# Optimization experiments

Measured on AMD Instinct MI355X. Metric: run time of the kernel, lower is better.

The kernel has to match this reference:

```python
import math
import jax, jax.numpy as jnp
from jax import lax
import numpy as np

B, M, L = 256, 21, 512
P, S, D = 16, 8, 256
NL, EXP, H, LAM = 3, 2, 96, 0.01
T = (L - P) // S + 1  # 63 patches
HID = D * EXP


def _pos_enc():
    pe = np.zeros((T, D), np.float32)
    pos = np.arange(T, dtype=np.float32)[:, None]
    div = np.exp(np.arange(0, D, 2, dtype=np.float32) * (-math.log(10000.0) / D))
    pe[:, 0::2] = np.sin(pos * div)
    pe[:, 1::2] = np.cos(pos * div)
    return jnp.asarray(pe)


def _clin(zr, zi, Wr, Wi, br, bi):
    # faithful to torch: bias br added to both terms of yr (cancels), bi added twice in yi
    yr = (zr @ Wr.T + br) - (zi @ Wi.T + br)
    yi = (zr @ Wi.T + bi) + (zi @ Wr.T + bi)
    return yr, yi


def _softshrink(zr, zi):
    mag = jnp.sqrt(zr * zr + zi * zi)
    scale = jnp.maximum(mag - LAM, 0.0) / (mag + 1e-8) * (mag > LAM).astype(zr.dtype)
    return zr * scale, zi * scale


def _layernorm(x, g, b):
    mu = jnp.mean(x, -1, keepdims=True)
    var = jnp.mean((x - mu) ** 2, -1, keepdims=True)
    return (x - mu) / jnp.sqrt(var + 1e-5) * g + b


def _block(x, p):
    (Tw, Tb, Gew, Geb, Gpw, Gpb,
     H1Wr, H1Wi, H1br, H1bi, H2Wr, H2Wi, H2br, H2bi, lng, lnb) = p
    g = jax.nn.gelu(x @ Gew.T + Geb, approximate=False) @ Gpw.T + Gpb
    zf = jnp.fft.rfft(x, axis=1)  # FFT along time/patch axis T
    zr, zi = zf.real, zf.imag
    zr, zi = _clin(zr, zi, H1Wr, H1Wi, H1br, H1bi)
    zr, zi = _softshrink(zr, zi)
    zr, zi = _clin(zr, zi, H2Wr, H2Wi, H2br, H2bi)
    pt = jnp.fft.irfft(lax.complex(zr, zi), n=x.shape[1], axis=1)
    out = (g * pt) @ Tw.T + Tb
    return _layernorm(out + x, lng, lnb)


def _forward(x, conv_w, conv_b, tp, sp, gate_w, gate_b, proj_w, proj_b):
    # per-instance, per-variable norm over time (biased std, eps on std)
    mean = jnp.mean(x, -1, keepdims=True)
    std = jnp.sqrt(jnp.mean((x - mean) ** 2, -1, keepdims=True))
    xn = (x - mean) / (std + 1e-5)
    patches = lax.conv_general_dilated(xn, conv_w, (S,), 'VALID',
                                       dimension_numbers=('NCH', 'OIH', 'NCH'))
    patches = patches + conv_b[None, :, None]
    h = patches.transpose(0, 2, 1) + _pos_enc()[None]  # (B, T, D)
    t = h
    s = h
    for i in range(NL):
        t = _block(t, tuple(a[i] for a in tp))
        s = _block(s, tuple(a[i] for a in sp))
    gate = jax.nn.sigmoid(t @ gate_w.T + gate_b)
    feat = gate * t + (1.0 - gate) * s
    out = feat.reshape(feat.shape[0], -1) @ proj_w.T + proj_b
    y = out.reshape(-1, M, H) * (std + 1e-5) + mean
    return y


def setup_inputs() -> dict:
    key = jax.random.key(0)
    ks = iter(jax.random.split(key, 64))

    def nrm(shape, scale):
        return jax.random.normal(next(ks), shape, jnp.float32) * scale

    inp = {'x': nrm((B, M, L), 1.0)}
    inp['conv_w'] = nrm((D, M, P), 1.0 / math.sqrt(M * P))
    inp['conv_b'] = jnp.zeros((D,), jnp.float32)

    def layer_params(prefix):
        d = {}
        d[prefix + 'Tw'] = nrm((NL, D, D), 1.0 / math.sqrt(D))
        d[prefix + 'Tb'] = jnp.zeros((NL, D), jnp.float32)
        d[prefix + 'Gew'] = nrm((NL, HID, D), 1.0 / math.sqrt(D))
        d[prefix + 'Geb'] = jnp.zeros((NL, HID), jnp.float32)
        d[prefix + 'Gpw'] = nrm((NL, D, HID), 1.0 / math.sqrt(HID))
        d[prefix + 'Gpb'] = jnp.zeros((NL, D), jnp.float32)
        for hname in ('H1', 'H2'):
            d[prefix + hname + 'Wr'] = nrm((NL, D, D), 1.0 / math.sqrt(D))
            d[prefix + hname + 'Wi'] = nrm((NL, D, D), 1.0 / math.sqrt(D))
            d[prefix + hname + 'br'] = jnp.zeros((NL, D), jnp.float32)
            d[prefix + hname + 'bi'] = jnp.zeros((NL, D), jnp.float32)
        d[prefix + 'lng'] = jnp.ones((NL, D), jnp.float32)
        d[prefix + 'lnb'] = jnp.zeros((NL, D), jnp.float32)
        return d

    inp.update(layer_params('t_'))
    inp.update(layer_params('s_'))
    inp['gate_w'] = nrm((1, D), 1.0 / math.sqrt(D))
    inp['gate_b'] = jnp.zeros((1,), jnp.float32)
    inp['proj_w'] = nrm((M * H, T * D), 1.0 / math.sqrt(T * D))
    inp['proj_b'] = jnp.zeros((M * H,), jnp.float32)
    return inp


def reference(x, conv_w, conv_b,
              t_Tw, t_Tb, t_Gew, t_Geb, t_Gpw, t_Gpb,
              t_H1Wr, t_H1Wi, t_H1br, t_H1bi, t_H2Wr, t_H2Wi, t_H2br, t_H2bi, t_lng, t_lnb,
              s_Tw, s_Tb, s_Gew, s_Geb, s_Gpw, s_Gpb,
              s_H1Wr, s_H1Wi, s_H1br, s_H1bi, s_H2Wr, s_H2Wi, s_H2br, s_H2bi, s_lng, s_lnb,
              gate_w, gate_b, proj_w, proj_b):
    tp = (t_Tw, t_Tb, t_Gew, t_Geb, t_Gpw, t_Gpb,
          t_H1Wr, t_H1Wi, t_H1br, t_H1bi, t_H2Wr, t_H2Wi, t_H2br, t_H2bi, t_lng, t_lnb)
    sp = (s_Tw, s_Tb, s_Gew, s_Geb, s_Gpw, s_Gpb,
          s_H1Wr, s_H1Wi, s_H1br, s_H1bi, s_H2Wr, s_H2Wi, s_H2br, s_H2bi, s_lng, s_lnb)
    return _forward(x, conv_w, conv_b, tp, sp, gate_w, gate_b, proj_w, proj_b)
```

## Files before the change

kernel.cpp:

```cpp
#include <hip/hip_runtime.h>
#include <cstddef>
#include <cstdint>

#define B_    256
#define M_    21
#define L_    512
#define D_    256
#define T_    63
#define F_    32
#define NT_   16128
#define HID_  512
#define KCP_  352
#define H_    96
#define LAM_  0.01f
#define PZ_   16

typedef __attribute__((ext_vector_type(8))) short short8;
typedef __attribute__((ext_vector_type(4))) float f32x4;
typedef unsigned int u32;
typedef const u32 __attribute__((address_space(1)))* gas1_t;
typedef u32 __attribute__((address_space(3)))* las3_t;

__device__ __forceinline__ void async_copy16(const void* g, void* l) {
  __builtin_amdgcn_global_load_lds((gas1_t)g, (las3_t)(uintptr_t)l, 16, 0, 0);
}
__device__ __forceinline__ unsigned short f2bf(float x) {
  unsigned u = __float_as_uint(x);
  return (unsigned short)((u + 0x7FFF + ((u >> 16) & 1)) >> 16);
}
__device__ __forceinline__ float bf2f(unsigned short u) {
  return __uint_as_float(((unsigned)u) << 16);
}
__device__ __forceinline__ float gelu_exact(float v) {
  return 0.5f * v * (1.0f + erff(v * 0.70710678118654752f));
}
__device__ __forceinline__ float block_sum256(float v, float* red4) {
  #pragma unroll
  for (int off = 32; off > 0; off >>= 1) v += __shfl_down(v, off, 64);
  if ((threadIdx.x & 63) == 0) red4[threadIdx.x >> 6] = v;
  __syncthreads();
  float r = red4[0] + red4[1] + red4[2] + red4[3];
  __syncthreads();
  return r;
}
__device__ __forceinline__ float wave_sum(float v) {
  #pragma unroll
  for (int off = 1; off < 64; off <<= 1) v += __shfl_xor(v, off, 64);
  return v;
}

struct CvtEnt { const float* src; unsigned short* dst; int rows, scol, dcol, blk0; };
struct CvtArgs { CvtEnt e[19]; int nent; };
__global__ __launch_bounds__(256) void wprep_kernel(CvtArgs a) {
  int blk = blockIdx.x, e = 0;
  while (e + 1 < a.nent && a.e[e + 1].blk0 <= blk) ++e;
  CvtEnt en = a.e[e];
  int idx = (blk - en.blk0) * 256 + threadIdx.x;
  int total = en.rows * en.dcol;
  if (idx >= total) return;
  int r = idx / en.dcol, c = idx - r * en.dcol;
  float v = (c < en.scol) ? en.src[(size_t)r * en.scol + c] : 0.f;
  en.dst[idx] = f2bf(v);
}

struct CatArgs { const float* wr[12]; const float* wi[12]; };
__global__ __launch_bounds__(256) void wcat_kernel(CatArgs a, unsigned short* dst) {
  int e = blockIdx.x >> 10;
  int idx = ((blockIdx.x & 1023) << 8) + threadIdx.x;
  int r = idx >> 9, c = idx & 511;
  int cp = r >> 1, p = r & 1, d = c >> 1, q = c & 1;
  const float* wr = a.wr[e];
  const float* wi = a.wi[e];
  float v;
  if (p == 0) v = (q == 0) ? wr[cp * 256 + d] : -wi[cp * 256 + d];
  else        v = (q == 0) ? wi[cp * 256 + d] :  wr[cp * 256 + d];
  dst[(size_t)e * 262144 + idx] = f2bf(v);
}

template <int ACT, int OUTBF, int BIASM, int KSTEPS, int CVTA, int CVTW,
          int SHRINK, int MULPT, int SPLITK, int BK, int RT>
__global__ __launch_bounds__(256) void mm_kernel(
    const void* __restrict__ Av,
    const unsigned short* __restrict__ W0, const unsigned short* __restrict__ W1,
    const float* __restrict__ Wf,
    const float* __restrict__ b0, const float* __restrict__ b1,
    const unsigned short* __restrict__ ptb,
    void* __restrict__ Cv,
    const int K, const int Dout, const int ksteps_rt, const int yhalf,
    const int prow, const int totk) {
  constexpr int NP = BK / 32;
  constexpr int RWS = 32 * RT;
  __shared__ __align__(16) unsigned short As[NP * RWS * 32];
  __shared__ __align__(16) unsigned short Bs[NP * 128 * 32];
  const int tid = threadIdx.x, w = tid >> 6, lane = tid & 63;
  const int quad = lane >> 4, r16 = lane & 15;
  int nks = KSTEPS ? KSTEPS : ksteps_rt;
  const int ksbeg = SPLITK ? (int)blockIdx.z * nks : 0;
  if (SPLITK) { int rem = totk - ksbeg; if (nks > rem) nks = rem; }
  const int kst = ksbeg * BK;
  const int tower = ((int)blockIdx.y >= yhalf) ? 1 : 0;
  const unsigned short* Wb = tower ? W1 : W0;
  const float* bias = tower ? b1 : b0;

  const unsigned short* Ab = (const unsigned short*)Av;
  const float* Af = (const float*)Av;
  const unsigned short* gA = nullptr;
  unsigned short* lA = As + (w * 8 * RT) * 32;
  if (!CVTA) gA = Ab + (size_t)((int)blockIdx.y * RWS + w * 8 * RT + (lane >> 2)) * K
                     + kst + (lane & 3) * 8;
  const unsigned short* gB = nullptr;
  unsigned short* lB = Bs + (w * 32) * 32;
  if (!CVTW) gB = Wb + (size_t)((int)blockIdx.x * 128 + w * 32 + (lane >> 2)) * K
                     + kst + (lane & 3) * 8;
  const int crow = tid >> 3;
  const int ck4  = (tid & 7) << 2;

  float4 areg[NP][RT];
  float4 wreg[NP][4];
  auto loadA = [&](int ksi) {
    #pragma unroll
    for (int p = 0; p < NP; ++p)
      #pragma unroll
      for (int rr = 0; rr < RT; ++rr)
        areg[p][rr] = *reinterpret_cast<const float4*>(
            Af + (size_t)((int)blockIdx.y * RWS + crow + 32 * rr) * K
               + kst + ksi * BK + p * 32 + ck4);
  };
  auto loadW = [&](int ksi) {
    #pragma unroll
    for (int p = 0; p < NP; ++p)
      #pragma unroll
      for (int rr = 0; rr < 4; ++rr) {
        int wrow = (int)blockIdx.x * 128 + crow + 32 * rr;
        if (wrow >= Dout) wrow = Dout - 1;
        wreg[p][rr] = *reinterpret_cast<const float4*>(
            Wf + (size_t)wrow * K + kst + ksi * BK + p * 32 + ck4);
      }
  };
  if (CVTA) loadA(0);
  if (CVTW) loadW(0);

  f32x4 acc[RT][4];
  #pragma unroll
  for (int i = 0; i < RT; ++i)
    #pragma unroll
    for (int j = 0; j < 4; ++j)
      #pragma unroll
      for (int r = 0; r < 4; ++r) acc[i][j][r] = 0.f;

  for (int ks = 0; ks < nks; ++ks) {
    if (!CVTA) {
      #pragma unroll
      for (int p = 0; p < NP; ++p)
        #pragma unroll
        for (int c = 0; c < RT / 2; ++c)
          async_copy16(gA + (size_t)(c * 16) * K + p * 32,
                       lA + p * (RWS * 32) + c * 16 * 32);
      gA += BK;
    } else {
      #pragma unroll
      for (int p = 0; p < NP; ++p)
        #pragma unroll
        for (int rr = 0; rr < RT; ++rr) {
          float4 v = areg[p][rr];
          ushort4 o; o.x = f2bf(v.x); o.y = f2bf(v.y); o.z = f2bf(v.z); o.w = f2bf(v.w);
          *reinterpret_cast<ushort4*>(As + p * (RWS * 32) + (crow + 32 * rr) * 32 + ck4) = o;
        }
    }
    if (!CVTW) {
      #pragma unroll
      for (int p = 0; p < NP; ++p) {
        async_copy16(gB + p * 32, lB + p * 4096);
        async_copy16(gB + (size_t)16 * K + p * 32, lB + p * 4096 + 16 * 32);
      }
      gB += BK;
    } else {
      #pragma unroll
      for (int p = 0; p < NP; ++p)
        #pragma unroll
        for (int rr = 0; rr < 4; ++rr) {
          float4 v = wreg[p][rr];
          ushort4 o; o.x = f2bf(v.x); o.y = f2bf(v.y); o.z = f2bf(v.z); o.w = f2bf(v.w);
          *reinterpret_cast<ushort4*>(Bs + p * 4096 + (crow + 32 * rr) * 32 + ck4) = o;
        }
    }
    __syncthreads();
    if (CVTA && ks + 1 < nks) loadA(ks + 1);
    if (CVTW && ks + 1 < nks) loadW(ks + 1);
    #pragma unroll
    for (int p = 0; p < NP; ++p) {
      const unsigned short* pa = As + p * (RWS * 32) + ((w >> 1) * 16 * RT + r16) * 32 + quad * 8;
      const unsigned short* pb = Bs + p * 4096 + (64 * (w & 1) + r16) * 32 + quad * 8;
      short8 af[RT], bfv[4];
      #pragma unroll
      for (int i = 0; i < RT; ++i) af[i] = *reinterpret_cast<const short8*>(pa + i * 512);
      #pragma unroll
      for (int j = 0; j < 4; ++j) bfv[j] = *reinterpret_cast<const short8*>(pb + j * 512);
      #pragma unroll
      for (int i = 0; i < RT; ++i)
        #pragma unroll
        for (int j = 0; j < 4; ++j)
          acc[i][j] = __builtin_amdgcn_mfma_f32_16x16x32_bf16(af[i], bfv[j], acc[i][j], 0, 0, 0);
    }
    __syncthreads();
  }

  float* Cf = (float*)Cv;
  unsigned short* Cb = (unsigned short*)Cv;
  if (SPLITK) Cf += (size_t)blockIdx.z * prow * Dout;
  const int colb = (int)blockIdx.x * 128 + 64 * (w & 1) + r16;
  const int rowb = (int)blockIdx.y * RWS + 16 * RT * (w >> 1) + quad * 4;
  #pragma unroll
  for (int j = 0; j < 4; ++j) {
    int col = colb + 16 * j;
    float bv = 0.f;
    if (BIASM == 0) bv = bias[col];
    else if (BIASM == 1) bv = (col & 1) ? 2.0f * bias[col >> 1] : 0.f;
    bool colok = (BIASM != 2) || (col < Dout);
    #pragma unroll
    for (int i = 0; i < RT; ++i) {
      #pragma unroll
      for (int r = 0; r < 4; ++r) {
        int row = rowb + 16 * i + r;
        float v = acc[i][j][r] + bv;
        if (ACT == 1) v = gelu_exact(v);
        if (SHRINK) {
          float o = __shfl_xor(v, 1, 64);
          float mag = sqrtf(v * v + o * o);
          float s = (mag > LAM_) ? (mag - LAM_) / (mag + 1e-8f) : 0.f;
          v *= s;
        }
        if (MULPT) v *= bf2f(ptb[(size_t)row * Dout + col]);
        if (colok) {
          if (OUTBF) Cb[(size_t)row * Dout + col] = f2bf(v);
          else       Cf[(size_t)row * Dout + col] = v;
        }
      }
    }
  }
}

__global__ __launch_bounds__(256) void norm_kernel(const float* __restrict__ x,
    float* __restrict__ xn, float* __restrict__ meanb, float* __restrict__ stdb) {
  __shared__ float red[4];
  int bm = blockIdx.x;
  const float* xr = x + (size_t)bm * L_;
  float v0 = xr[threadIdx.x], v1 = xr[threadIdx.x + 256];
  float mu = block_sum256(v0 + v1, red) * (1.0f / L_);
  float d0 = v0 - mu, d1 = v1 - mu;
  float sd = sqrtf(block_sum256(d0 * d0 + d1 * d1, red) * (1.0f / L_));
  float inv = 1.0f / (sd + 1e-5f);
  float* xo = xn + (size_t)bm * L_;
  xo[threadIdx.x] = d0 * inv;
  xo[threadIdx.x + 256] = d1 * inv;
  if (threadIdx.x == 0) { meanb[bm] = mu; stdb[bm] = sd; }
}

__global__ __launch_bounds__(256) void im2col_kernel(const float* __restrict__ xn,
                                                     unsigned short* __restrict__ im) {
  int row = blockIdx.x;
  int b = row / T_, t = row - b * T_;
  const float* xb = xn + (size_t)b * M_ * L_ + t * 8;
  unsigned short* o = im + (size_t)row * KCP_;
  for (int i = threadIdx.x; i < KCP_; i += 256) {
    float v = 0.f;
    if (i < 336) { int m = i >> 4, p = i & 15; v = xb[m * L_ + p]; }
    o[i] = f2bf(v);
  }
}

__global__ __launch_bounds__(256) void add_pe_kernel(const float* __restrict__ g0,
                                                     float* __restrict__ x32) {
  int row = blockIdx.x, d = threadIdx.x;
  int t = row % T_;
  size_t idx = (size_t)row * D_ + d;
  float freq = expf((float)(d & ~1) * (-9.210340371976184f / 256.0f));
  float ang = (float)t * freq;
  float pe = (d & 1) ? cosf(ang) : sinf(ang);
  float h = g0[idx] + pe;
  x32[idx] = h;
  x32[idx + (size_t)NT_ * D_] = h;
}

__global__ __launch_bounds__(256) void dft_kernel(const float* __restrict__ X,
                                                  unsigned short* __restrict__ Zcat) {
  __shared__ float2 tw[T_ * F_];
  int bt = blockIdx.x, d = threadIdx.x;
  for (int i = threadIdx.x; i < T_ * F_; i += 256) {
    int t = i >> 5, f = i & 31;
    int k = (f * t) % T_;
    float sn, cs;
    sincosf((6.283185307179586f / 63.0f) * (float)k, &sn, &cs);
    tw[i] = make_float2(cs, -sn);
  }
  __syncthreads();
  const float* xb = X + (size_t)bt * T_ * D_ + d;
  float ar[F_], ai[F_];
  #pragma unroll
  for (int f = 0; f < F_; ++f) { ar[f] = 0.f; ai[f] = 0.f; }
  for (int t = 0; t < T_; ++t) {
    float v = xb[(size_t)t * D_];
    const float2* w = &tw[t * F_];
    #pragma unroll
    for (int f = 0; f < F_; ++f) {
      float2 c = w[f];
      ar[f] = fmaf(v, c.x, ar[f]);
      ai[f] = fmaf(v, c.y, ai[f]);
    }
  }
  u32* z = reinterpret_cast<u32*>(Zcat + (size_t)bt * F_ * 512);
  #pragma unroll
  for (int f = 0; f < F_; ++f)
    z[f * 256 + d] = (u32)f2bf(ar[f]) | ((u32)f2bf(ai[f]) << 16);
}

__global__ __launch_bounds__(256) void irfft_kernel(const unsigned short* __restrict__ Y,
                                                    unsigned short* __restrict__ ptb) {
  __shared__ float2 tw[T_ * 31];
  int bt = blockIdx.x, d = threadIdx.x;
  for (int i = threadIdx.x; i < T_ * 31; i += 256) {
    int t = i / 31, f = i - t * 31 + 1;
    int k = (f * t) % T_;
    float sn, cs;
    sincosf((6.283185307179586f / 63.0f) * (float)k, &sn, &cs);
    tw[i] = make_float2(cs * (2.0f / 63.0f), -sn * (2.0f / 63.0f));
  }
  __syncthreads();
  const unsigned short* yb = Y + (size_t)bt * F_ * 512 + 2 * d;
  float y0 = bf2f(yb[0]) * (1.0f / 63.0f);
  float yr[31], yi[31];
  #pragma unroll
  for (int f = 1; f < F_; ++f) {
    u32 p = *reinterpret_cast<const u32*>(yb + (size_t)f * 512);
    yr[f - 1] = bf2f((unsigned short)(p & 0xffff));
    yi[f - 1] = bf2f((unsigned short)(p >> 16));
  }
  unsigned short* po = ptb + (size_t)bt * T_ * D_ + d;
  for (int t = 0; t < T_; ++t) {
    const float2* w = &tw[t * 31];
    float acc0 = y0, acc1 = 0.f;
    #pragma unroll
    for (int f = 0; f < 31; f += 2) {
      float2 c = w[f];
      acc0 = fmaf(yr[f], c.x, fmaf(yi[f], c.y, acc0));
      if (f + 1 < 31) {
        float2 c1 = w[f + 1];
        acc1 = fmaf(yr[f + 1], c1.x, fmaf(yi[f + 1], c1.y, acc1));
      }
    }
    po[(size_t)t * D_] = f2bf(acc0 + acc1);
  }
}

__global__ __launch_bounds__(256) void ln_kernel(const float* __restrict__ outb,
    float* __restrict__ x, const float* __restrict__ g0, const float* __restrict__ b0,
    const float* __restrict__ g1, const float* __restrict__ b1, int yhalf) {
  int row = blockIdx.x * 4 + (threadIdx.x >> 6);
  int lane = threadIdx.x & 63;
  const float* g = (row >= yhalf) ? g1 : g0;
  const float* b = (row >= yhalf) ? b1 : b0;
  size_t base = (size_t)row * D_ + lane * 4;
  float4 ov = *reinterpret_cast<const float4*>(outb + base);
  float4 xv = *reinterpret_cast<const float4*>(x + base);
  float v0 = ov.x + xv.x, v1 = ov.y + xv.y, v2 = ov.z + xv.z, v3 = ov.w + xv.w;
  float mu = wave_sum(v0 + v1 + v2 + v3) * (1.0f / D_);
  v0 -= mu; v1 -= mu; v2 -= mu; v3 -= mu;
  float var = wave_sum(v0 * v0 + v1 * v1 + v2 * v2 + v3 * v3) * (1.0f / D_);
  float is = rsqrtf(var + 1e-5f);
  float4 gv = *reinterpret_cast<const float4*>(g + lane * 4);
  float4 bv = *reinterpret_cast<const float4*>(b + lane * 4);
  float4 o;
  o.x = v0 * is * gv.x + bv.x;
  o.y = v1 * is * gv.y + bv.y;
  o.z = v2 * is * gv.z + bv.z;
  o.w = v3 * is * gv.w + bv.w;
  *reinterpret_cast<float4*>(x + base) = o;
}

__global__ __launch_bounds__(256) void gate_feat_kernel(const float* __restrict__ x32,
    const float* __restrict__ gw, const float* __restrict__ gb,
    unsigned short* __restrict__ featbf) {
  int row = blockIdx.x * 4 + (threadIdx.x >> 6);
  int lane = threadIdx.x & 63;
  size_t base = (size_t)row * D_ + lane * 4;
  float4 tv = *reinterpret_cast<const float4*>(x32 + base);
  float4 sv = *reinterpret_cast<const float4*>(x32 + base + (size_t)NT_ * D_);
  float4 gv = *reinterpret_cast<const float4*>(gw + lane * 4);
  float dot = wave_sum(tv.x * gv.x + tv.y * gv.y + tv.z * gv.z + tv.w * gv.w) + gb[0];
  float gate = 1.0f / (1.0f + expf(-dot));
  ushort4 o;
  o.x = f2bf(gate * tv.x + (1.0f - gate) * sv.x);
  o.y = f2bf(gate * tv.y + (1.0f - gate) * sv.y);
  o.z = f2bf(gate * tv.z + (1.0f - gate) * sv.z);
  o.w = f2bf(gate * tv.w + (1.0f - gate) * sv.w);
  *reinterpret_cast<ushort4*>(featbf + base) = o;
}

__global__ __launch_bounds__(256) void final_kernel(const float* __restrict__ part,
    const float* __restrict__ pb, const float* __restrict__ stdb,
    const float* __restrict__ meanb, float* __restrict__ y) {
  int i = blockIdx.x * 256 + threadIdx.x;
  float acc = 0.f;
  #pragma unroll
  for (int z = 0; z < PZ_; ++z) acc += part[(size_t)z * 516096 + i];
  int b = i / 2016;
  int col = i - b * 2016;
  int m = col / H_;
  float sc = stdb[b * M_ + m] + 1e-5f;
  y[i] = (acc + pb[col]) * sc + meanb[b * M_ + m];
}

extern "C" void kernel_launch(void* const* d_in, const int* in_sizes, int n_in,
                              void* d_out, int out_size, void* d_ws, size_t ws_size,
                              hipStream_t stream) {
  const float* x      = (const float*)d_in[0];
  const float* conv_w = (const float*)d_in[1];
  const float* conv_b = (const float*)d_in[2];
  const float* tP[16];
  const float* sP[16];
  for (int i = 0; i < 16; ++i) tP[i] = (const float*)d_in[3 + i];
  for (int i = 0; i < 16; ++i) sP[i] = (const float*)d_in[19 + i];
  const float* gate_w = (const float*)d_in[35];
  const float* gate_b = (const float*)d_in[36];
  const float* proj_w = (const float*)d_in[37];
  const float* proj_b = (const float*)d_in[38];
  float* out = (float*)d_out;

  float* ws    = (float*)d_ws;
  float* x32   = ws;
  unsigned short* wb = (unsigned short*)(x32 + 8257536);
  float* meanb = x32 + 8257536 + 2600960;
  float* stdb  = meanb + 5376;
  float* R1    = stdb + 5376 + 16;
  float* R2    = R1 + 8388608;

  unsigned short* im2colB = (unsigned short*)R1;
  unsigned short* Zcat    = (unsigned short*)R1;
  unsigned short* Ycat1   = (unsigned short*)(R1 + 4194304);
  unsigned short* ptb     = (unsigned short*)(R1 + 4194304);
  unsigned short* gp      = (unsigned short*)R1;
  unsigned short* featbf  = (unsigned short*)R1;

  float* xn     = R2;
  float* g0buf  = R2;
  unsigned short* Ycat2b = (unsigned short*)R2;
  unsigned short* hidB = (unsigned short*)R2;
  float* outb   = R2;
  float* part   = R2;

  unsigned short* convW = wb;
  unsigned short* sets  = wb + 90112;
  unsigned short* catW  = wb + 90112 + 1966080;

  CvtArgs ca; int blk0 = 0, ne = 0;
  auto add_ent = [&](const float* s, unsigned short* d, int rows, int scol, int dcol) {
    ca.e[ne].src = s; ca.e[ne].dst = d; ca.e[ne].rows = rows;
    ca.e[ne].scol = scol; ca.e[ne].dcol = dcol; ca.e[ne].blk0 = blk0;
    blk0 += (rows * dcol + 255) / 256; ++ne;
  };
  add_ent(conv_w, convW, 256, 336, 352);
  for (int tw = 0; tw < 2; ++tw) {
    const float** Pp = tw ? (const float**)sP : (const float**)tP;
    for (int l = 0; l < 3; ++l) {
      unsigned short* sb = sets + (size_t)(tw * 3 + l) * 327680;
      add_ent(Pp[2] + (size_t)l * 131072, sb,          512, 256, 256);
      add_ent(Pp[4] + (size_t)l * 131072, sb + 131072, 256, 512, 512);
      add_ent(Pp[0] + (size_t)l * 65536,  sb + 262144, 256, 256, 256);
    }
  }
  ca.nent = ne;
  wprep_kernel<<<blk0, 256, 0, stream>>>(ca);

  CatArgs cat;
  for (int tw = 0; tw < 2; ++tw) {
    const float** Pp = tw ? (const float**)sP : (const float**)tP;
    for (int l = 0; l < 3; ++l) {
      int e0 = (tw * 3 + l) * 2;
      cat.wr[e0]     = Pp[6]  + (size_t)l * 65536;
      cat.wi[e0]     = Pp[7]  + (size_t)l * 65536;
      cat.wr[e0 + 1] = Pp[10] + (size_t)l * 65536;
      cat.wi[e0 + 1] = Pp[11] + (size_t)l * 65536;
    }
  }
  wcat_kernel<<<12 * 1024, 256, 0, stream>>>(cat, catW);

  norm_kernel<<<B_ * M_, 256, 0, stream>>>(x, xn, meanb, stdb);
  im2col_kernel<<<NT_, 256, 0, stream>>>(xn, im2colB);
  mm_kernel<0, 0, 0, 11, 0, 0, 0, 0, 0, 32, 2><<<dim3(2, 252), 256, 0, stream>>>(
      im2colB, convW, convW, nullptr, conv_b, conv_b, nullptr, g0buf,
      KCP_, 256, 0, 1 << 30, 0, 0);
  add_pe_kernel<<<NT_, 256, 0, stream>>>(g0buf, x32);

  for (int l = 0; l < 3; ++l) {
    unsigned short* st0 = sets + (size_t)l * 327680;
    unsigned short* st1 = sets + (size_t)(3 + l) * 327680;
    unsigned short* c1t0 = catW + (size_t)((0 + l) * 2) * 262144;
    unsigned short* c2t0 = c1t0 + 262144;
    unsigned short* c1t1 = catW + (size_t)((3 + l) * 2) * 262144;
    unsigned short* c2t1 = c1t1 + 262144;

    dft_kernel<<<2 * B_, 256, 0, stream>>>(x32, Zcat);
    mm_kernel<0, 1, 1, 8, 0, 0, 1, 0, 0, 64, 2><<<dim3(4, 256), 256, 0, stream>>>(
        Zcat, c1t0, c1t1, nullptr, tP[9] + (size_t)l * D_, sP[9] + (size_t)l * D_,
        nullptr, Ycat1, 512, 512, 0, 128, 0, 0);
    mm_kernel<0, 1, 1, 8, 0, 0, 0, 0, 0, 64, 2><<<dim3(4, 256), 256, 0, stream>>>(
        Ycat1, c2t0, c2t1, nullptr, tP[13] + (size_t)l * D_, sP[13] + (size_t)l * D_,
        nullptr, Ycat2b, 512, 512, 0, 128, 0, 0);
    irfft_kernel<<<2 * B_, 256, 0, stream>>>(Ycat2b, ptb);
    mm_kernel<1, 1, 0, 4, 1, 0, 0, 0, 0, 64, 2><<<dim3(4, 504), 256, 0, stream>>>(
        x32, st0, st1, nullptr, tP[3] + (size_t)l * HID_, sP[3] + (size_t)l * HID_,
        nullptr, hidB, 256, 512, 0, 252, 0, 0);
    mm_kernel<0, 1, 0, 8, 0, 0, 0, 1, 0, 64, 2><<<dim3(2, 504), 256, 0, stream>>>(
        hidB, st0 + 131072, st1 + 131072, nullptr,
        tP[5] + (size_t)l * D_, sP[5] + (size_t)l * D_, ptb, gp, 512, 256, 0, 252, 0, 0);
    mm_kernel<0, 0, 0, 4, 0, 0, 0, 0, 0, 64, 2><<<dim3(2, 504), 256, 0, stream>>>(
        gp, st0 + 262144, st1 + 262144, nullptr,
        tP[1] + (size_t)l * D_, sP[1] + (size_t)l * D_, nullptr, outb, 256, 256, 0, 252, 0, 0);
    ln_kernel<<<2 * NT_ / 4, 256, 0, stream>>>(outb, x32,
        tP[14] + (size_t)l * D_, tP[15] + (size_t)l * D_,
        sP[14] + (size_t)l * D_, sP[15] + (size_t)l * D_, NT_);
  }

  gate_feat_kernel<<<NT_ / 4, 256, 0, stream>>>(x32, gate_w, gate_b, featbf);
  mm_kernel<0, 0, 2, 0, 0, 1, 0, 0, 1, 64, 2><<<dim3(16, 4, PZ_), 256, 0, stream>>>(
      featbf, nullptr, nullptr, proj_w, nullptr, nullptr, nullptr, part,
      NT_, 2016, 16, 1 << 30, 256, 252);
  final_kernel<<<2016, 256, 0, stream>>>(part, proj_b, stdb, meanb, out);
}
```

Measured before the change: 995.2 us.

## Add dedicated register-prefetched split-K projection kernel with on-the-fly weight bf16 conversion

Replaces the generic mm_kernel for the final projection (256 x 16128 times 16128 x 2016) with a specialized kernel. It double-buffers LDS, prefetches the next A and fp32 weight tiles into registers while MFMA runs on the current tile, and converts the weights to bf16 while storing them to LDS. The split-K factor drops from 16 to 12 slices of 21 k-steps each. This is meant to hide global-load latency on the large weight stream. The cost is higher register pressure and a custom barrier that waits only on LDS counters.

New measurement: 1.020 ms. +2.5%, slower.

```diff
diff --git a/kernel.cpp b/kernel.cpp
--- a/kernel.cpp
+++ b/kernel.cpp
@@ -13,7 +13,8 @@
 #define KCP_  352
 #define H_    96
 #define LAM_  0.01f
-#define PZ_   16
+#define PZ_   12
+#define PKN_  21
 
 typedef __attribute__((ext_vector_type(8))) short short8;
 typedef __attribute__((ext_vector_type(4))) float f32x4;
@@ -33,6 +34,9 @@
 }
 __device__ __forceinline__ float gelu_exact(float v) {
   return 0.5f * v * (1.0f + erff(v * 0.70710678118654752f));
+}
+__device__ __forceinline__ void bar_sync() {
+  asm volatile("s_waitcnt lgkmcnt(0)\ns_barrier" ::: "memory");
 }
 __device__ __forceinline__ float block_sum256(float v, float* red4) {
   #pragma unroll
@@ -240,6 +244,116 @@
   }
 }
 
+__global__ __launch_bounds__(256) void proj_kernel(
+    const unsigned short* __restrict__ A, const float* __restrict__ Wf,
+    float* __restrict__ part) {
+  __shared__ __align__(16) unsigned short As[2][4096];
+  __shared__ __align__(16) unsigned short Bs[2][8192];
+  const int tid = threadIdx.x, w = tid >> 6, lane = tid & 63;
+  const int quad = lane >> 4, r16 = lane & 15;
+  const int bx = blockIdx.x, by = blockIdx.y, bz = blockIdx.z;
+  const int kst = bz * (PKN_ * 64);
+
+  const int ar = tid >> 2, ac0 = (tid & 3) << 4;
+  const unsigned short* gA = A + (size_t)(by * 64 + ar) * NT_ + kst + ac0;
+  unsigned short* dA0 = &As[0][(ac0 >> 5) * 2048 + ar * 32 + (ac0 & 31)];
+  unsigned short* dA1 = &As[1][(ac0 >> 5) * 2048 + ar * 32 + (ac0 & 31)];
+  const int wr0 = tid >> 3, wc4 = (tid & 7) << 2;
+  const float* gWr[4];
+  #pragma unroll
+  for (int rr = 0; rr < 4; ++rr) {
+    int r = bx * 128 + wr0 + 32 * rr;
+    if (r > 2015) r = 2015;
+    gWr[rr] = Wf + (size_t)r * NT_ + kst + wc4;
+  }
+
+  float4 rA0[2], rA1[2];
+  float4 rW0[2][4], rW1[2][4];
+  auto loadA = [&](int ksi, float4 (&ra)[2]) {
+    #pragma unroll
+    for (int c = 0; c < 2; ++c)
+      ra[c] = *reinterpret_cast<const float4*>(gA + ksi * 64 + c * 8);
+  };
+  auto loadW = [&](int ksi, float4 (&rw)[2][4]) {
+    #pragma unroll
+    for (int p = 0; p < 2; ++p)
+      #pragma unroll
+      for (int rr = 0; rr < 4; ++rr)
+        rw[p][rr] = *reinterpret_cast<const float4*>(gWr[rr] + ksi * 64 + p * 32);
+  };
+  auto storeA = [&](float4 (&ra)[2], unsigned short* dA) {
+    *reinterpret_cast<float4*>(dA) = ra[0];
+    *reinterpret_cast<float4*>(dA + 8) = ra[1];
+  };
+  auto storeW = [&](float4 (&rw)[2][4], int buf) {
+    #pragma unroll
+    for (int p = 0; p < 2; ++p)
+      #pragma unroll
+      for (int rr = 0; rr < 4; ++rr) {
+        float4 v = rw[p][rr];
+        ushort4 o; o.x = f2bf(v.x); o.y = f2bf(v.y); o.z = f2bf(v.z); o.w = f2bf(v.w);
+        *reinterpret_cast<ushort4*>(&Bs[buf][p * 4096 + (wr0 + 32 * rr) * 32 + wc4]) = o;
+      }
+  };
+
+  f32x4 acc[2][4];
+  #pragma unroll
+  for (int i = 0; i < 2; ++i)
+    #pragma unroll
+    for (int j = 0; j < 4; ++j)
+      #pragma unroll
+      for (int r = 0; r < 4; ++r) acc[i][j][r] = 0.f;
+
+  auto compute = [&](int buf) {
+    #pragma unroll
+    for (int p = 0; p < 2; ++p) {
+      const unsigned short* pa = &As[buf][p * 2048 + ((w >> 1) * 32 + r16) * 32 + quad * 8];
+      const unsigned short* pb = &Bs[buf][p * 4096 + ((w & 1) * 64 + r16) * 32 + quad * 8];
+      short8 af[2], bfv[4];
+      #pragma unroll
+      for (int i = 0; i < 2; ++i) af[i] = *reinterpret_cast<const short8*>(pa + i * 512);
+      #pragma unroll
+      for (int j = 0; j < 4; ++j) bfv[j] = *reinterpret_cast<const short8*>(pb + j * 512);
+      #pragma unroll
+      for (int i = 0; i < 2; ++i)
+        #pragma unroll
+        for (int j = 0; j < 4; ++j)
+          acc[i][j] = __builtin_amdgcn_mfma_f32_16x16x32_bf16(af[i], bfv[j], acc[i][j], 0, 0, 0);
+    }
+  };
+
+  loadA(0, rA0); loadW(0, rW0);
+  loadA(1, rA1); loadW(1, rW1);
+  storeA(rA0, dA0); storeW(rW0, 0);
+  bar_sync();
+
+  for (int ks = 0; ks < PKN_ - 1; ks += 2) {
+    if (ks + 2 < PKN_) { loadA(ks + 2, rA0); loadW(ks + 2, rW0); }
+    storeA(rA1, dA1); storeW(rW1, 1);
+    compute(0);
+    bar_sync();
+    if (ks + 3 < PKN_) { loadA(ks + 3, rA1); loadW(ks + 3, rW1); }
+    storeA(rA0, dA0); storeW(rW0, 0);
+    compute(1);
+    bar_sync();
+  }
+  compute(0);
+
+  float* Cf = part + (size_t)bz * 256 * 2016;
+  const int colb = bx * 128 + 64 * (w & 1) + r16;
+  const int rowb = by * 64 + 32 * (w >> 1) + quad * 4;
+  #pragma unroll
+  for (int j = 0; j < 4; ++j) {
+    int col = colb + 16 * j;
+    if (col >= 2016) continue;
+    #pragma unroll
+    for (int i = 0; i < 2; ++i)
+      #pragma unroll
+      for (int r = 0; r < 4; ++r)
+        Cf[(size_t)(rowb + 16 * i + r) * 2016 + col] = acc[i][j][r];
+  }
+}
+
 __global__ __launch_bounds__(256) void norm_kernel(const float* __restrict__ x,
     float* __restrict__ xn, float* __restrict__ meanb, float* __restrict__ stdb) {
   __shared__ float red[4];
@@ -522,8 +636,6 @@
   }
 
   gate_feat_kernel<<<NT_ / 4, 256, 0, stream>>>(x32, gate_w, gate_b, featbf);
-  mm_kernel<0, 0, 2, 0, 0, 1, 0, 0, 1, 64, 2><<<dim3(16, 4, PZ_), 256, 0, stream>>>(
-      featbf, nullptr, nullptr, proj_w, nullptr, nullptr, nullptr, part,
-      NT_, 2016, 16, 1 << 30, 256, 252);
+  proj_kernel<<<dim3(16, 4, PZ_), 256, 0, stream>>>(featbf, proj_w, part);
   final_kernel<<<2016, 256, 0, stream>>>(part, proj_b, stdb, meanb, out);
 }
```

## Double-buffer LDS tiles in GEMM kernel to overlap staging with MFMA compute

Applied to the files above, without the earlier changes.

Shared-memory A and B tiles are duplicated into two buffers. The next k-step's tile is staged (async copy or converted register data) into the alternate buffer while MFMAs run on the current one. This leaves one barrier per k-step instead of two. It doubles LDS usage per block, which may lower occupancy, and relies on async loads completing by the barrier.

After: 1.020 ms. 1.03x slower.

```diff
diff --git a/kernel.cpp b/kernel.cpp
--- a/kernel.cpp
+++ b/kernel.cpp
@@ -90,8 +90,10 @@
     const int prow, const int totk) {
   constexpr int NP = BK / 32;
   constexpr int RWS = 32 * RT;
-  __shared__ __align__(16) unsigned short As[NP * RWS * 32];
-  __shared__ __align__(16) unsigned short Bs[NP * 128 * 32];
+  constexpr int ASZ = NP * RWS * 32;
+  constexpr int BSZ = NP * 128 * 32;
+  __shared__ __align__(16) unsigned short As[2][ASZ];
+  __shared__ __align__(16) unsigned short Bs[2][BSZ];
   const int tid = threadIdx.x, w = tid >> 6, lane = tid & 63;
   const int quad = lane >> 4, r16 = lane & 15;
   int nks = KSTEPS ? KSTEPS : ksteps_rt;
@@ -105,11 +107,9 @@
   const unsigned short* Ab = (const unsigned short*)Av;
   const float* Af = (const float*)Av;
   const unsigned short* gA = nullptr;
-  unsigned short* lA = As + (w * 8 * RT) * 32;
   if (!CVTA) gA = Ab + (size_t)((int)blockIdx.y * RWS + w * 8 * RT + (lane >> 2)) * K
                      + kst + (lane & 3) * 8;
   const unsigned short* gB = nullptr;
-  unsigned short* lB = Bs + (w * 32) * 32;
   if (!CVTW) gB = Wb + (size_t)((int)blockIdx.x * 128 + w * 32 + (lane >> 2)) * K
                      + kst + (lane & 3) * 8;
   const int crow = tid >> 3;
@@ -137,26 +137,14 @@
             Wf + (size_t)wrow * K + kst + ksi * BK + p * 32 + ck4);
       }
   };
-  if (CVTA) loadA(0);
-  if (CVTW) loadW(0);
-
-  f32x4 acc[RT][4];
-  #pragma unroll
-  for (int i = 0; i < RT; ++i)
-    #pragma unroll
-    for (int j = 0; j < 4; ++j)
-      #pragma unroll
-      for (int r = 0; r < 4; ++r) acc[i][j][r] = 0.f;
-
-  for (int ks = 0; ks < nks; ++ks) {
+  auto stageA = [&](int ksi, int buf) {
     if (!CVTA) {
       #pragma unroll
       for (int p = 0; p < NP; ++p)
         #pragma unroll
         for (int c = 0; c < RT / 2; ++c)
-          async_copy16(gA + (size_t)(c * 16) * K + p * 32,
-                       lA + p * (RWS * 32) + c * 16 * 32);
-      gA += BK;
+          async_copy16(gA + (size_t)ksi * BK + (size_t)(c * 16) * K + p * 32,
+                       &As[buf][(w * 8 * RT) * 32 + p * (RWS * 32) + c * 16 * 32]);
     } else {
       #pragma unroll
       for (int p = 0; p < NP; ++p)
@@ -164,16 +152,19 @@
         for (int rr = 0; rr < RT; ++rr) {
           float4 v = areg[p][rr];
           ushort4 o; o.x = f2bf(v.x); o.y = f2bf(v.y); o.z = f2bf(v.z); o.w = f2bf(v.w);
-          *reinterpret_cast<ushort4*>(As + p * (RWS * 32) + (crow + 32 * rr) * 32 + ck4) = o;
+          *reinterpret_cast<ushort4*>(&As[buf][p * (RWS * 32) + (crow + 32 * rr) * 32 + ck4]) = o;
         }
     }
+  };
+  auto stageW = [&](int ksi, int buf) {
     if (!CVTW) {
       #pragma unroll
       for (int p = 0; p < NP; ++p) {
-        async_copy16(gB + p * 32, lB + p * 4096);
-        async_copy16(gB + (size_t)16 * K + p * 32, lB + p * 4096 + 16 * 32);
+        async_copy16(gB + (size_t)ksi * BK + p * 32,
+                     &Bs[buf][(w * 32) * 32 + p * 4096]);
+        async_copy16(gB + (size_t)ksi * BK + (size_t)16 * K + p * 32,
+                     &Bs[buf][(w * 32) * 32 + p * 4096 + 16 * 32]);
       }
-      gB += BK;
     } else {
       #pragma unroll
       for (int p = 0; p < NP; ++p)
@@ -181,16 +172,24 @@
         for (int rr = 0; rr < 4; ++rr) {
           float4 v = wreg[p][rr];
           ushort4 o; o.x = f2bf(v.x); o.y = f2bf(v.y); o.z = f2bf(v.z); o.w = f2bf(v.w);
-          *reinterpret_cast<ushort4*>(Bs + p * 4096 + (crow + 32 * rr) * 32 + ck4) = o;
+          *reinterpret_cast<ushort4*>(&Bs[buf][p * 4096 + (crow + 32 * rr) * 32 + ck4]) = o;
         }
     }
-    __syncthreads();
-    if (CVTA && ks + 1 < nks) loadA(ks + 1);
-    if (CVTW && ks + 1 < nks) loadW(ks + 1);
+  };
+
+  f32x4 acc[RT][4];
+  #pragma unroll
+  for (int i = 0; i < RT; ++i)
+    #pragma unroll
+    for (int j = 0; j < 4; ++j)
+      #pragma unroll
+      for (int r = 0; r < 4; ++r) acc[i][j][r] = 0.f;
+
+  auto compute = [&](int buf) {
     #pragma unroll
     for (int p = 0; p < NP; ++p) {
-      const unsigned short* pa = As + p * (RWS * 32) + ((w >> 1) * 16 * RT + r16) * 32 + quad * 8;
-      const unsigned short* pb = Bs + p * 4096 + (64 * (w & 1) + r16) * 32 + quad * 8;
+      const unsigned short* pa = &As[buf][p * (RWS * 32) + ((w >> 1) * 16 * RT + r16) * 32 + quad * 8];
+      const unsigned short* pb = &Bs[buf][p * 4096 + (64 * (w & 1) + r16) * 32 + quad * 8];
       short8 af[RT], bfv[4];
       #pragma unroll
       for (int i = 0; i < RT; ++i) af[i] = *reinterpret_cast<const short8*>(pa + i * 512);
@@ -202,7 +201,27 @@
         for (int j = 0; j < 4; ++j)
           acc[i][j] = __builtin_amdgcn_mfma_f32_16x16x32_bf16(af[i], bfv[j], acc[i][j], 0, 0, 0);
     }
+  };
+
+  if (CVTA) loadA(0);
+  if (CVTW) loadW(0);
+  stageA(0, 0);
+  stageW(0, 0);
+  if (CVTA && nks > 1) loadA(1);
+  if (CVTW && nks > 1) loadW(1);
+  __syncthreads();
+
+  int buf = 0;
+  for (int ks = 0; ks < nks; ++ks) {
+    if (ks + 1 < nks) {
+      stageA(ks + 1, buf ^ 1);
+      stageW(ks + 1, buf ^ 1);
+      if (CVTA && ks + 2 < nks) loadA(ks + 2);
+      if (CVTW && ks + 2 < nks) loadW(ks + 2);
+    }
+    compute(buf);
     __syncthreads();
+    buf ^= 1;
   }
 
   float* Cf = (float*)Cv;
```

## Fuse positional encoding into conv GEMM and LayerNorm into Tw GEMM epilogue

Applied to the files above, without the earlier changes.

Adds a PEW epilogue mode to the generic GEMM that adds the sinusoidal positional encoding and writes both tower copies, removing the separate add_pe kernel. Replaces the Tw projection GEMM plus the standalone LayerNorm kernel with a new twln_kernel. Each block computes a full 64x256 row tile, adds bias and residual, reduces mean and variance across waves through LDS, and writes the normalized result in place. This removes the fp32 intermediate round trip and two launches per layer, at the cost of a wide-N tile with larger register use and a single-pass variance formula.

New measurement: 984.0 us. No clear change (-1.1%).

```diff
diff --git a/kernel.cpp b/kernel.cpp
--- a/kernel.cpp
+++ b/kernel.cpp
@@ -78,7 +78,7 @@
 }
 
 template <int ACT, int OUTBF, int BIASM, int KSTEPS, int CVTA, int CVTW,
-          int SHRINK, int MULPT, int SPLITK, int BK, int RT>
+          int SHRINK, int MULPT, int SPLITK, int BK, int RT, int PEW>
 __global__ __launch_bounds__(256) void mm_kernel(
     const void* __restrict__ Av,
     const unsigned short* __restrict__ W0, const unsigned short* __restrict__ W1,
@@ -232,12 +232,145 @@
         }
         if (MULPT) v *= bf2f(ptb[(size_t)row * Dout + col]);
         if (colok) {
-          if (OUTBF) Cb[(size_t)row * Dout + col] = f2bf(v);
-          else       Cf[(size_t)row * Dout + col] = v;
+          if (PEW) {
+            int t = row % T_;
+            float freq = expf((float)(col & ~1) * (-9.210340371976184f / 256.0f));
+            float ang = (float)t * freq;
+            float pe = (col & 1) ? cosf(ang) : sinf(ang);
+            float h = v + pe;
+            Cf[(size_t)row * Dout + col] = h;
+            Cf[(size_t)row * Dout + col + (size_t)NT_ * D_] = h;
+          } else if (OUTBF) {
+            Cb[(size_t)row * Dout + col] = f2bf(v);
+          } else {
+            Cf[(size_t)row * Dout + col] = v;
+          }
         }
       }
     }
   }
+}
+
+__global__ __launch_bounds__(256) void twln_kernel(
+    const unsigned short* __restrict__ A,
+    const unsigned short* __restrict__ W0, const unsigned short* __restrict__ W1,
+    const float* __restrict__ b0, const float* __restrict__ b1,
+    const float* __restrict__ lg0, const float* __restrict__ lb0,
+    const float* __restrict__ lg1, const float* __restrict__ lb1,
+    float* __restrict__ x32) {
+  __shared__ __align__(16) unsigned short As[2][64 * 32];
+  __shared__ __align__(16) unsigned short Bs[2][256 * 32];
+  const int tid = threadIdx.x, w = tid >> 6, lane = tid & 63;
+  const int quad = lane >> 4, r16 = lane & 15;
+  const int rh = w >> 1, ch = w & 1;
+  const int by = blockIdx.x;
+  const int tower = (by >= 252) ? 1 : 0;
+  const unsigned short* W = tower ? W1 : W0;
+  const float* bias = tower ? b1 : b0;
+  const float* lng = tower ? lg1 : lg0;
+  const float* lnb = tower ? lb1 : lb0;
+
+  const unsigned short* gA = A + (size_t)(by * 64 + (tid >> 2)) * 256 + (tid & 3) * 8;
+  const unsigned short* gW = W + (size_t)(tid >> 2) * 256 + (tid & 3) * 8;
+
+  f32x4 acc[2][8];
+  #pragma unroll
+  for (int i = 0; i < 2; ++i)
+    #pragma unroll
+    for (int j = 0; j < 8; ++j)
+      #pragma unroll
+      for (int r = 0; r < 4; ++r) acc[i][j][r] = 0.f;
+
+  for (int ks = 0; ks < 4; ++ks) {
+    #pragma unroll
+    for (int p = 0; p < 2; ++p)
+      async_copy16(gA + p * 32, (char*)As + p * 4096 + tid * 16);
+    #pragma unroll
+    for (int p = 0; p < 2; ++p)
+      #pragma unroll
+      for (int k = 0; k < 4; ++k)
+        async_copy16(gW + (size_t)k * 16384 + p * 32,
+                     (char*)Bs + p * 16384 + k * 4096 + tid * 16);
+    gA += 64; gW += 64;
+    __syncthreads();
+    #pragma unroll
+    for (int p = 0; p < 2; ++p) {
+      const unsigned short* pa = As[p] + (rh * 32 + r16) * 32 + quad * 8;
+      const unsigned short* pb = Bs[p] + (ch * 128 + r16) * 32 + quad * 8;
+      short8 af[2], bfv[8];
+      #pragma unroll
+      for (int i = 0; i < 2; ++i) af[i] = *reinterpret_cast<const short8*>(pa + i * 512);
+      #pragma unroll
+      for (int j = 0; j < 8; ++j) bfv[j] = *reinterpret_cast<const short8*>(pb + j * 512);
+      #pragma unroll
+      for (int i = 0; i < 2; ++i)
+        #pragma unroll
+        for (int j = 0; j < 8; ++j)
+          acc[i][j] = __builtin_amdgcn_mfma_f32_16x16x32_bf16(af[i], bfv[j], acc[i][j], 0, 0, 0);
+    }
+    __syncthreads();
+  }
+
+  const int rowb = by * 64 + rh * 32 + quad * 4;
+  const int colb = ch * 128 + r16;
+  float s[2][4], sq[2][4];
+  #pragma unroll
+  for (int i = 0; i < 2; ++i)
+    #pragma unroll
+    for (int r = 0; r < 4; ++r) { s[i][r] = 0.f; sq[i][r] = 0.f; }
+  #pragma unroll
+  for (int j = 0; j < 8; ++j) {
+    int col = colb + j * 16;
+    float bv = bias[col];
+    #pragma unroll
+    for (int i = 0; i < 2; ++i)
+      #pragma unroll
+      for (int r = 0; r < 4; ++r) {
+        int row = rowb + i * 16 + r;
+        float h = acc[i][j][r] + bv + x32[(size_t)row * 256 + col];
+        acc[i][j][r] = h;
+        s[i][r] += h;
+        sq[i][r] += h * h;
+      }
+  }
+  #pragma unroll
+  for (int off = 1; off < 16; off <<= 1)
+    #pragma unroll
+    for (int i = 0; i < 2; ++i)
+      #pragma unroll
+      for (int r = 0; r < 4; ++r) {
+        s[i][r]  += __shfl_xor(s[i][r],  off, 64);
+        sq[i][r] += __shfl_xor(sq[i][r], off, 64);
+      }
+  float* red = (float*)As;
+  if (r16 == 0) {
+    #pragma unroll
+    for (int i = 0; i < 2; ++i)
+      #pragma unroll
+      for (int r = 0; r < 4; ++r) {
+        int lr = rh * 32 + i * 16 + quad * 4 + r;
+        red[lr * 4 + ch * 2]     = s[i][r];
+        red[lr * 4 + ch * 2 + 1] = sq[i][r];
+      }
+  }
+  __syncthreads();
+  #pragma unroll
+  for (int i = 0; i < 2; ++i)
+    #pragma unroll
+    for (int r = 0; r < 4; ++r) {
+      int lr = rh * 32 + i * 16 + quad * 4 + r;
+      float tot = red[lr * 4] + red[lr * 4 + 2];
+      float tsq = red[lr * 4 + 1] + red[lr * 4 + 3];
+      float mu = tot * (1.0f / 256.0f);
+      float var = tsq * (1.0f / 256.0f) - mu * mu;
+      float is = rsqrtf(var + 1e-5f);
+      int row = rowb + i * 16 + r;
+      #pragma unroll
+      for (int j = 0; j < 8; ++j) {
+        int col = colb + j * 16;
+        x32[(size_t)row * 256 + col] = (acc[i][j][r] - mu) * is * lng[col] + lnb[col];
+      }
+    }
 }
 
 __global__ __launch_bounds__(256) void norm_kernel(const float* __restrict__ x,
@@ -269,19 +402,6 @@
   }
 }
 
-__global__ __launch_bounds__(256) void add_pe_kernel(const float* __restrict__ g0,
-                                                     float* __restrict__ x32) {
-  int row = blockIdx.x, d = threadIdx.x;
-  int t = row % T_;
-  size_t idx = (size_t)row * D_ + d;
-  float freq = expf((float)(d & ~1) * (-9.210340371976184f / 256.0f));
-  float ang = (float)t * freq;
-  float pe = (d & 1) ? cosf(ang) : sinf(ang);
-  float h = g0[idx] + pe;
-  x32[idx] = h;
-  x32[idx + (size_t)NT_ * D_] = h;
-}
-
 __global__ __launch_bounds__(256) void dft_kernel(const float* __restrict__ X,
                                                   unsigned short* __restrict__ Zcat) {
   __shared__ float2 tw[T_ * F_];
@@ -350,31 +470,6 @@
     }
     po[(size_t)t * D_] = f2bf(acc0 + acc1);
   }
-}
-
-__global__ __launch_bounds__(256) void ln_kernel(const float* __restrict__ outb,
-    float* __restrict__ x, const float* __restrict__ g0, const float* __restrict__ b0,
-    const float* __restrict__ g1, const float* __restrict__ b1, int yhalf) {
-  int row = blockIdx.x * 4 + (threadIdx.x >> 6);
-  int lane = threadIdx.x & 63;
-  const float* g = (row >= yhalf) ? g1 : g0;
-  const float* b = (row >= yhalf) ? b1 : b0;
-  size_t base = (size_t)row * D_ + lane * 4;
-  float4 ov = *reinterpret_cast<const float4*>(outb + base);
-  float4 xv = *reinterpret_cast<const float4*>(x + base);
-  float v0 = ov.x + xv.x, v1 = ov.y + xv.y, v2 = ov.z + xv.z, v3 = ov.w + xv.w;
-  float mu = wave_sum(v0 + v1 + v2 + v3) * (1.0f / D_);
-  v0 -= mu; v1 -= mu; v2 -= mu; v3 -= mu;
-  float var = wave_sum(v0 * v0 + v1 * v1 + v2 * v2 + v3 * v3) * (1.0f / D_);
-  float is = rsqrtf(var + 1e-5f);
-  float4 gv = *reinterpret_cast<const float4*>(g + lane * 4);
-  float4 bv = *reinterpret_cast<const float4*>(b + lane * 4);
-  float4 o;
-  o.x = v0 * is * gv.x + bv.x;
-  o.y = v1 * is * gv.y + bv.y;
-  o.z = v2 * is * gv.z + bv.z;
-  o.w = v3 * is * gv.w + bv.w;
-  *reinterpret_cast<float4*>(x + base) = o;
 }
 
 __global__ __launch_bounds__(256) void gate_feat_kernel(const float* __restrict__ x32,
@@ -442,10 +537,8 @@
   unsigned short* featbf  = (unsigned short*)R1;
 
   float* xn     = R2;
-  float* g0buf  = R2;
   unsigned short* Ycat2b = (unsigned short*)R2;
   unsigned short* hidB = (unsigned short*)R2;
-  float* outb   = R2;
   float* part   = R2;
 
   unsigned short* convW = wb;
@@ -486,10 +579,9 @@
 
   norm_kernel<<<B_ * M_, 256, 0, stream>>>(x, xn, meanb, stdb);
   im2col_kernel<<<NT_, 256, 0, stream>>>(xn, im2colB);
-  mm_kernel<0, 0, 0, 11, 0, 0, 0, 0, 0, 32, 2><<<dim3(2, 252), 256, 0, stream>>>(
-      im2colB, convW, convW, nullptr, conv_b, conv_b, nullptr, g0buf,
+  mm_kernel<0, 0, 0, 11, 0, 0, 0, 0, 0, 32, 2, 1><<<dim3(2, 252), 256, 0, stream>>>(
+      im2colB, convW, convW, nullptr, conv_b, conv_b, nullptr, x32,
       KCP_, 256, 0, 1 << 30, 0, 0);
-  add_pe_kernel<<<NT_, 256, 0, stream>>>(g0buf, x32);
 
   for (int l = 0; l < 3; ++l) {
     unsigned short* st0 = sets + (size_t)l * 327680;
@@ -500,29 +592,28 @@
     unsigned short* c2t1 = c1t1 + 262144;
 
     dft_kernel<<<2 * B_, 256, 0, stream>>>(x32, Zcat);
-    mm_kernel<0, 1, 1, 8, 0, 0, 1, 0, 0, 64, 2><<<dim3(4, 256), 256, 0, stream>>>(
+    mm_kernel<0, 1, 1, 8, 0, 0, 1, 0, 0, 64, 2, 0><<<dim3(4, 256), 256, 0, stream>>>(
         Zcat, c1t0, c1t1, nullptr, tP[9] + (size_t)l * D_, sP[9] + (size_t)l * D_,
         nullptr, Ycat1, 512, 512, 0, 128, 0, 0);
-    mm_kernel<0, 1, 1, 8, 0, 0, 0, 0, 0, 64, 2><<<dim3(4, 256), 256, 0, stream>>>(
+    mm_kernel<0, 1, 1, 8, 0, 0, 0, 0, 0, 64, 2, 0><<<dim3(4, 256), 256, 0, stream>>>(
         Ycat1, c2t0, c2t1, nullptr, tP[13] + (size_t)l * D_, sP[13] + (size_t)l * D_,
         nullptr, Ycat2b, 512, 512, 0, 128, 0, 0);
     irfft_kernel<<<2 * B_, 256, 0, stream>>>(Ycat2b, ptb);
-    mm_kernel<1, 1, 0, 4, 1, 0, 0, 0, 0, 64, 2><<<dim3(4, 504), 256, 0, stream>>>(
+    mm_kernel<1, 1, 0, 4, 1, 0, 0, 0, 0, 64, 2, 0><<<dim3(4, 504), 256, 0, stream>>>(
         x32, st0, st1, nullptr, tP[3] + (size_t)l * HID_, sP[3] + (size_t)l * HID_,
         nullptr, hidB, 256, 512, 0, 252, 0, 0);
-    mm_kernel<0, 1, 0, 8, 0, 0, 0, 1, 0, 64, 2><<<dim3(2, 504), 256, 0, stream>>>(
+    mm_kernel<0, 1, 0, 8, 0, 0, 0, 1, 0, 64, 2, 0><<<dim3(2, 504), 256, 0, stream>>>(
         hidB, st0 + 131072, st1 + 131072, nullptr,
         tP[5] + (size_t)l * D_, sP[5] + (size_t)l * D_, ptb, gp, 512, 256, 0, 252, 0, 0);
-    mm_kernel<0, 0, 0, 4, 0, 0, 0, 0, 0, 64, 2><<<dim3(2, 504), 256, 0, stream>>>(
-        gp, st0 + 262144, st1 + 262144, nullptr,
-        tP[1] + (size_t)l * D_, sP[1] + (size_t)l * D_, nullptr, outb, 256, 256, 0, 252, 0, 0);
-    ln_kernel<<<2 * NT_ / 4, 256, 0, stream>>>(outb, x32,
+    twln_kernel<<<504, 256, 0, stream>>>(
+        gp, st0 + 262144, st1 + 262144,
+        tP[1] + (size_t)l * D_, sP[1] + (size_t)l * D_,
         tP[14] + (size_t)l * D_, tP[15] + (size_t)l * D_,
-        sP[14] + (size_t)l * D_, sP[15] + (size_t)l * D_, NT_);
+        sP[14] + (size_t)l * D_, sP[15] + (size_t)l * D_, x32);
   }
 
   gate_feat_kernel<<<NT_ / 4, 256, 0, stream>>>(x32, gate_w, gate_b, featbf);
-  mm_kernel<0, 0, 2, 0, 0, 1, 0, 0, 1, 64, 2><<<dim3(16, 4, PZ_), 256, 0, stream>>>(
+  mm_kernel<0, 0, 2, 0, 0, 1, 0, 0, 1, 64, 2, 0><<<dim3(16, 4, PZ_), 256, 0, stream>>>(
       featbf, nullptr, nullptr, proj_w, nullptr, nullptr, nullptr, part,
       NT_, 2016, 16, 1 << 30, 256, 252);
   final_kernel<<<2016, 256, 0, stream>>>(part, proj_b, stdb, meanb, out);
```
